# Optimization experiments

Hardware: AMD Instinct MI355X
Metric: run time of the kernel (lower is better)

Reference implementation:

```python
import jax, jax.numpy as jnp
import numpy as np

H = 8
NUM_GRAPHS = 128
EDGE_DIM = 147

def _glorot(k, shape, fan_in):
    return jax.random.normal(k, shape, jnp.float32) * (1.0 / np.sqrt(fan_in))

def setup_inputs():
    ks = jax.random.split(jax.random.key(0), 28)
    N, E = 50000, 200000
    inp = {}
    inp['x'] = jax.random.normal(ks[0], (N, 64), jnp.float32)
    inp['edge_attr'] = jax.random.uniform(ks[1], (E, EDGE_DIM), dtype=jnp.float32)
    dims = [(64, 64), (512, 64), (512, 32)]  # (in_channels, per-head out) per GATConv layer
    ki = 2
    for i in range(3):
        cin, c = dims[i]
        hc = H * c
        inp['W%d' % i] = _glorot(ks[ki], (hc, cin), cin); ki += 1
        inp['We%d' % i] = _glorot(ks[ki], (hc, EDGE_DIM), EDGE_DIM); ki += 1
        inp['as%d' % i] = _glorot(ks[ki], (1, H, c), c); ki += 1
        inp['ad%d' % i] = _glorot(ks[ki], (1, H, c), c); ki += 1
        inp['ae%d' % i] = _glorot(ks[ki], (1, H, c), c); ki += 1
        inp['b%d' % i] = jnp.zeros((hc,), jnp.float32); ki += 1
    inp['Wc'] = _glorot(ks[ki], (32, 256), 256)
    inp['bc'] = jnp.zeros((32,), jnp.float32)
    inp['edge_index'] = jax.random.randint(ks[ki + 1], (2, E), 0, N)
    inp['batch'] = jnp.sort(jax.random.randint(ks[ki + 2], (N,), 0, NUM_GRAPHS))
    return inp

def _gat_layer(x, src, dst, ea, W, We, a_s, a_d, a_e, b):
    # PyG GATConv (concat=True, eval mode): project, per-edge attention logits,
    # softmax over incoming edges of each destination node, weighted scatter-sum, bias.
    N = x.shape[0]
    HC = W.shape[0]
    C = HC // H
    xp = (x @ W.T).reshape(N, H, C)              # [N,H,C]
    ep = (ea @ We.T).reshape(-1, H, C)           # [E,H,C]
    logits = (xp * a_s).sum(-1)[src] + (xp * a_d).sum(-1)[dst] + (ep * a_e).sum(-1)
    logits = jax.nn.leaky_relu(logits, 0.2)      # [E,H]
    mx = jax.ops.segment_max(logits, dst, num_segments=N)
    mx = jnp.where(jnp.isfinite(mx), mx, 0.0)
    ex = jnp.exp(logits - mx[dst])
    denom = jax.ops.segment_sum(ex, dst, num_segments=N)
    attn = ex / (denom[dst] + 1e-16)             # [E,H]
    out = jax.ops.segment_sum(xp[src] * attn[:, :, None], dst, num_segments=N)
    return out.reshape(N, HC) + b

def _forward(x, edge_attr, params, Wc, bc, edge_index, batch):
    N = x.shape[0]
    src, dst = edge_index[0], edge_index[1]
    # GATConv add_self_loops=True, fill_value='mean': self-loop edge attr is
    # the per-node mean of incoming edge attrs (0 for isolated nodes).
    ones_e = jnp.ones((src.shape[0],), x.dtype)
    deg = jax.ops.segment_sum(ones_e, dst, num_segments=N)
    loop_attr = jax.ops.segment_sum(edge_attr, dst, num_segments=N) / jnp.clip(deg, 1.0)[:, None]
    ar = jnp.arange(N)
    src_f = jnp.concatenate([src, ar])
    dst_f = jnp.concatenate([dst, ar])
    ea_f = jnp.concatenate([edge_attr, loop_attr], axis=0)
    h = x
    for i, p in enumerate(params):
        h = _gat_layer(h, src_f, dst_f, ea_f, *p)
        if i < len(params) - 1:
            h = jax.nn.elu(h)  # dropout is identity in eval
    # batch indices are sorted and contiguous, so the unique->contiguous remap
    # in the original forward is the identity; global mean pool:
    cnt = jax.ops.segment_sum(jnp.ones((N,), h.dtype), batch, num_segments=NUM_GRAPHS)
    pooled = jax.ops.segment_sum(h, batch, num_segments=NUM_GRAPHS) / jnp.clip(cnt, 1.0)[:, None]
    return pooled @ Wc.T + bc

def reference(x, edge_attr, W0, We0, as0, ad0, ae0, b0, W1, We1, as1, ad1, ae1, b1, W2, We2, as2, ad2, ae2, b2, Wc, bc, edge_index, batch):
    params = [(W0, We0, as0, ad0, ae0, b0), (W1, We1, as1, ad1, ae1, b1), (W2, We2, as2, ad2, ae2, b2)]
    return _forward(x, edge_attr, params, Wc, bc, edge_index, batch)
```

## Files before the change

kernel.cpp:

```cpp
#include <hip/hip_runtime.h>
#include <hip/hip_bf16.h>
#include <math.h>

typedef __attribute__((ext_vector_type(8))) _Float16 f16x8;
typedef __attribute__((ext_vector_type(4))) _Float16 f16x4;
typedef __attribute__((ext_vector_type(4))) float f32x4;

#define AS1(p) ((const __attribute__((address_space(1))) void*)(p))
#define AS3(p) ((__attribute__((address_space(3))) void*)(p))

__device__ __forceinline__ float leaky02(float x){ return x > 0.f ? x : 0.2f*x; }
__device__ __forceinline__ ushort f2h(float f){ _Float16 h = (_Float16)f; return *(ushort*)&h; }
__device__ __forceinline__ float h2f(ushort u){ _Float16 h = *(_Float16*)&u; return (float)h; }

__global__ void count_kernel(const int* __restrict__ dst, int* __restrict__ cnt, int E){
  int e = blockIdx.x*blockDim.x + threadIdx.x;
  if (e < E) atomicAdd(&cnt[dst[e]], 1);
}

__global__ void scanA_kernel(const int* __restrict__ cnt, int* __restrict__ bsum, int N){
  __shared__ int sd[256];
  int i = blockIdx.x*256 + threadIdx.x;
  sd[threadIdx.x] = (i<N) ? cnt[i] : 0;
  __syncthreads();
  for (int off=128; off>0; off>>=1){
    if (threadIdx.x < off) sd[threadIdx.x] += sd[threadIdx.x+off];
    __syncthreads();
  }
  if (threadIdx.x==0) bsum[blockIdx.x] = sd[0];
}
__global__ void scanB_kernel(int* __restrict__ bsum, int B){
  __shared__ int sd[256];
  int t = threadIdx.x;
  int v = (t<B) ? bsum[t] : 0;
  sd[t] = v;
  __syncthreads();
  for (int off=1; off<256; off<<=1){
    int u = (t>=off) ? sd[t-off] : 0;
    __syncthreads();
    sd[t] += u;
    __syncthreads();
  }
  if (t<B) bsum[t] = sd[t] - v;
}
__global__ void scanC_kernel(const int* __restrict__ cnt, const int* __restrict__ bsum,
                             int* __restrict__ row_ptr, int N){
  __shared__ int sd[256];
  int i = blockIdx.x*256 + threadIdx.x;
  int v = (i<N) ? cnt[i] : 0;
  sd[threadIdx.x] = v;
  __syncthreads();
  for (int off=1; off<256; off<<=1){
    int u = (threadIdx.x>=off) ? sd[threadIdx.x-off] : 0;
    __syncthreads();
    sd[threadIdx.x] += u;
    __syncthreads();
  }
  if (i < N) row_ptr[i+1] = sd[threadIdx.x] + bsum[blockIdx.x];
  if (i == 0) row_ptr[0] = 0;
}

__global__ void scatter_kernel(const int* __restrict__ dst, const int* __restrict__ row_ptr,
                               int* __restrict__ cursor, int* __restrict__ csr, int E){
  int e = blockIdx.x*blockDim.x + threadIdx.x;
  if (e < E){
    int d = dst[e];
    int pos = row_ptr[d] + atomicAdd(&cursor[d], 1);
    csr[pos] = e;
  }
}

__global__ void conv4_kernel(const float* __restrict__ p0, const float* __restrict__ p1,
                             const float* __restrict__ p2, const float* __restrict__ p3,
                             ushort* __restrict__ q0, ushort* __restrict__ q1,
                             ushort* __restrict__ q2, ushort* __restrict__ q3,
                             int n0, int n1, int n2, int n3){
  int i = blockIdx.x*256 + threadIdx.x;
  const float* src; ushort* dst; int loc;
  if (i < n0){ src=p0; dst=q0; loc=i; }
  else if (i < n0+n1){ src=p1; dst=q1; loc=i-n0; }
  else if (i < n0+n1+n2){ src=p2; dst=q2; loc=i-n0-n1; }
  else if (i < n0+n1+n2+n3){ src=p3; dst=q3; loc=i-n0-n1-n2; }
  else return;
  float4 v = reinterpret_cast<const float4*>(src)[loc];
  ushort4 o; o.x=f2h(v.x); o.y=f2h(v.y); o.z=f2h(v.z); o.w=f2h(v.w);
  reinterpret_cast<ushort4*>(dst)[loc] = o;
}

__global__ void wfold_direct_kernel(const float* __restrict__ We0, const float* __restrict__ ae0,
                                    const float* __restrict__ We1, const float* __restrict__ ae1,
                                    const float* __restrict__ We2, const float* __restrict__ ae2,
                                    ushort* __restrict__ Bh){
  int t = blockIdx.x*256 + threadIdx.x;
  if (t >= 32*160) return;
  int j = t/160, d = t%160;
  float s = 0.f;
  if (j < 24 && d < 147){
    int l = j >> 3, h = j & 7;
    const float* We = (l==0) ? We0 : (l==1) ? We1 : We2;
    const float* ae = (l==0) ? ae0 : (l==1) ? ae1 : ae2;
    int C = (l==2) ? 32 : 64;
    for (int c=0;c<C;c++) s = fmaf(We[(size_t)(h*C+c)*147 + d], ae[h*C+c], s);
  }
  Bh[t] = f2h(s);
}

__global__ __launch_bounds__(256) void edge_alpha_mfma_kernel(const float* __restrict__ ea, const ushort* __restrict__ Bh,
                                                              float* __restrict__ alphaE, int E){
  int wave = threadIdx.x>>6, lane = threadIdx.x&63;
  int fr = lane&15, fq = lane>>4;
  int m0 = blockIdx.x*64 + wave*16;
  f32x4 acc0 = {0.f,0.f,0.f,0.f}, acc1 = {0.f,0.f,0.f,0.f};
  int row = m0 + fr; if (row > E-1) row = E-1;
  const float*  ar = ea + (size_t)row*147;
  const ushort* b0 = Bh + (size_t)fr*160      + fq*8;
  const ushort* b1 = Bh + (size_t)(16+fr)*160 + fq*8;
  #pragma unroll
  for (int k=0;k<160;k+=32){
    int c0 = k + fq*8;
    f16x8 a;
    #pragma unroll
    for (int u=0;u<8;u++){
      float v = (c0+u < 147) ? ar[c0+u] : 0.f;
      a[u] = (_Float16)v;
    }
    f16x8 p = *(const f16x8*)(b0 + k);
    f16x8 q = *(const f16x8*)(b1 + k);
    acc0 = __builtin_amdgcn_mfma_f32_16x16x32_f16(a, p, acc0, 0, 0, 0);
    acc1 = __builtin_amdgcn_mfma_f32_16x16x32_f16(a, q, acc1, 0, 0, 0);
  }
  #pragma unroll
  for (int j=0;j<4;j++){
    int r = m0 + fq*4 + j;
    if (r < E){
      alphaE[(size_t)r*24 + fr] = acc0[j];
      if (fr < 8) alphaE[(size_t)r*24 + 16 + fr] = acc1[j];
    }
  }
}

__global__ __launch_bounds__(192) void loop_alpha_all_kernel(const float* __restrict__ alphaE, const int* __restrict__ row_ptr,
                                                             const int* __restrict__ csr, float* __restrict__ loopAE, int N){
  int n = blockIdx.x*8 + threadIdx.x/24;
  int j = threadIdx.x%24;
  if (n >= N) return;
  int row = row_ptr[n], end = row_ptr[n+1];
  float s = 0.f;
  for (int i=row;i<end;i++) s += alphaE[(size_t)csr[i]*24 + j];
  loopAE[(size_t)n*24 + j] = s / fmaxf((float)(end-row), 1.0f);
}

template<int CPH>
__global__ __launch_bounds__(256) void gemm_mfma_kernel(const ushort* __restrict__ A, const ushort* __restrict__ B,
                                                        ushort* __restrict__ C,
                                                        const float* __restrict__ a_s, const float* __restrict__ a_d,
                                                        float* __restrict__ alphaS, float* __restrict__ alphaD,
                                                        int M, int Nn, int K){
  __shared__ ushort As[128*64];
  __shared__ ushort Bs[128*64];
  int m0 = blockIdx.x*128, n0 = blockIdx.y*128;
  int wave = threadIdx.x >> 6, lane = threadIdx.x & 63;
  int wr = wave >> 1, wc = wave & 1;
  f32x4 acc[4][4];
  #pragma unroll
  for (int m=0;m<4;m++)
    #pragma unroll
    for (int n=0;n<4;n++) acc[m][n] = (f32x4){0.f,0.f,0.f,0.f};

  int lrow = lane >> 3;
  int lcol = lane & 7;
  int srcChunk = lcol ^ lrow;
  int fr = lane & 15;
  int fq = lane >> 4;

  for (int k0=0; k0<K; k0+=64){
    #pragma unroll
    for (int q=0;q<4;q++){
      int r = q*32 + wave*8 + lrow;
      int gr = m0 + r; if (gr > M-1) gr = M-1;
      __builtin_amdgcn_global_load_lds(AS1(A + (size_t)gr*K + k0 + srcChunk*8), AS3(&As[(q*32 + wave*8)*64]), 16, 0, 0);
      __builtin_amdgcn_global_load_lds(AS1(B + (size_t)(n0 + r)*K + k0 + srcChunk*8), AS3(&Bs[(q*32 + wave*8)*64]), 16, 0, 0);
    }
    __syncthreads();
    #pragma unroll
    for (int kk=0; kk<64; kk+=32){
      f16x8 a[4], b[4];
      #pragma unroll
      for (int m=0;m<4;m++){
        int Ra = wr*64 + m*16 + fr;
        int ch = ((kk>>3) + fq) ^ (Ra & 7);
        a[m] = *(const f16x8*)&As[Ra*64 + ch*8];
      }
      #pragma unroll
      for (int n=0;n<4;n++){
        int Rb = wc*64 + n*16 + fr;
        int ch = ((kk>>3) + fq) ^ (Rb & 7);
        b[n] = *(const f16x8*)&Bs[Rb*64 + ch*8];
      }
      #pragma unroll
      for (int m=0;m<4;m++)
        #pragma unroll
        for (int n=0;n<4;n++)
          acc[m][n] = __builtin_amdgcn_mfma_f32_16x16x32_f16(a[m], b[n], acc[m][n], 0, 0, 0);
    }
    __syncthreads();
  }
  #pragma unroll
  for (int m=0;m<4;m++){
    #pragma unroll
    for (int j=0;j<4;j++){
      int row = m0 + wr*64 + m*16 + fq*4 + j;
      if (row < M){
        ushort* cp = C + (size_t)row*Nn + n0 + wc*64 + fr;
        #pragma unroll
        for (int n=0;n<4;n++) cp[n*16] = f2h(acc[m][n][j]);
      }
    }
  }
  int colbase = n0 + wc*64;
  if (CPH == 64){
    int head = colbase >> 6;
    float asv[4], adv[4];
    #pragma unroll
    for (int n=0;n<4;n++){ int cih = n*16 + fr; asv[n] = a_s[head*64 + cih]; adv[n] = a_d[head*64 + cih]; }
    #pragma unroll
    for (int m=0;m<4;m++){
      float ps[4] = {0,0,0,0}, pd[4] = {0,0,0,0};
      #pragma unroll
      for (int n=0;n<4;n++)
        #pragma unroll
        for (int j=0;j<4;j++){ ps[j] = fmaf(acc[m][n][j], asv[n], ps[j]); pd[j] = fmaf(acc[m][n][j], adv[n], pd[j]); }
      #pragma unroll
      for (int off=1; off<16; off<<=1)
        #pragma unroll
        for (int j=0;j<4;j++){ ps[j] += __shfl_xor(ps[j], off); pd[j] += __shfl_xor(pd[j], off); }
      if (fr == 0){
        #pragma unroll
        for (int j=0;j<4;j++){
          int row = m0 + wr*64 + m*16 + fq*4 + j;
          if (row < M){ alphaS[(size_t)row*8 + head] = ps[j]; alphaD[(size_t)row*8 + head] = pd[j]; }
        }
      }
    }
  } else {
    int head0 = colbase >> 5;
    float asv[4], adv[4];
    #pragma unroll
    for (int n=0;n<4;n++){
      int h = head0 + (n>>1);
      int cih = (n&1)*16 + fr;
      asv[n] = a_s[h*32 + cih]; adv[n] = a_d[h*32 + cih];
    }
    #pragma unroll
    for (int m=0;m<4;m++){
      float psA[4]={0,0,0,0}, pdA[4]={0,0,0,0}, psB[4]={0,0,0,0}, pdB[4]={0,0,0,0};
      #pragma unroll
      for (int j=0;j<4;j++){
        #pragma unroll
        for (int n=0;n<2;n++){ psA[j] = fmaf(acc[m][n][j], asv[n], psA[j]); pdA[j] = fmaf(acc[m][n][j], adv[n], pdA[j]); }
        #pragma unroll
        for (int n=2;n<4;n++){ psB[j] = fmaf(acc[m][n][j], asv[n], psB[j]); pdB[j] = fmaf(acc[m][n][j], adv[n], pdB[j]); }
      }
      #pragma unroll
      for (int off=1; off<16; off<<=1)
        #pragma unroll
        for (int j=0;j<4;j++){
          psA[j] += __shfl_xor(psA[j], off); pdA[j] += __shfl_xor(pdA[j], off);
          psB[j] += __shfl_xor(psB[j], off); pdB[j] += __shfl_xor(pdB[j], off);
        }
      if (fr == 0){
        #pragma unroll
        for (int j=0;j<4;j++){
          int row = m0 + wr*64 + m*16 + fq*4 + j;
          if (row < M){
            alphaS[(size_t)row*8 + head0]     = psA[j]; alphaD[(size_t)row*8 + head0]     = pdA[j];
            alphaS[(size_t)row*8 + head0 + 1] = psB[j]; alphaD[(size_t)row*8 + head0 + 1] = pdB[j];
          }
        }
      }
    }
  }
}

template<int HC, int ELU>
__global__ __launch_bounds__(256) void aggregate_kernel(
    const ushort* __restrict__ xh, const float* __restrict__ alphaS, const float* __restrict__ alphaD,
    const float* __restrict__ alphaE, const float* __restrict__ loopAE,
    const int* __restrict__ row_ptr, const int* __restrict__ csr, const int* __restrict__ src,
    const float* __restrict__ bias, ushort* __restrict__ out, int N){
  constexpr int V = HC/64;
  int n = blockIdx.x*4 + (threadIdx.x>>6);
  if (n >= N) return;
  int lane = threadIdx.x & 63;
  int h = lane >> 3;
  float adn = alphaD[(size_t)n*8 + h];
  float ls = leaky02(alphaS[(size_t)n*8 + h] + adn + loopAE[(size_t)n*24 + h]);
  float ex = __expf(ls);
  float denom = ex;
  float acc[V];
  {
    const ushort* xr = xh + (size_t)n*HC + V*lane;
    if (V == 8){
      f16x8 v = *(const f16x8*)xr;
      #pragma unroll
      for (int j=0;j<8;j++) acc[j] = ex * (float)v[j];
    } else {
      f16x4 v = *(const f16x4*)xr;
      #pragma unroll
      for (int j=0;j<V;j++) acc[j] = ex * (float)v[j];
    }
  }
  int i1 = row_ptr[n+1];
  for (int i=row_ptr[n]; i<i1; i++){
    int e = csr[i]; int s = src[e];
    float t = leaky02(alphaS[(size_t)s*8 + h] + adn + alphaE[(size_t)e*24 + h]);
    float exv = __expf(t);
    denom += exv;
    const ushort* xs = xh + (size_t)s*HC + V*lane;
    if (V == 8){
      f16x8 v = *(const f16x8*)xs;
      #pragma unroll
      for (int j=0;j<8;j++) acc[j] = fmaf(exv, (float)v[j], acc[j]);
    } else {
      f16x4 v = *(const f16x4*)xs;
      #pragma unroll
      for (int j=0;j<V;j++) acc[j] = fmaf(exv, (float)v[j], acc[j]);
    }
  }
  float inv = 1.f/(denom + 1e-16f);
  if (V == 8){
    f16x8 ov;
    #pragma unroll
    for (int j=0;j<8;j++){
      float o = acc[j]*inv + bias[V*lane + j];
      if (ELU) o = (o > 0.f) ? o : expm1f(o);
      ov[j] = (_Float16)o;
    }
    *(f16x8*)(out + (size_t)n*HC + V*lane) = ov;
  } else {
    f16x4 ov;
    #pragma unroll
    for (int j=0;j<V;j++){
      float o = acc[j]*inv + bias[V*lane + j];
      if (ELU) o = (o > 0.f) ? o : expm1f(o);
      ov[j] = (_Float16)o;
    }
    *(f16x4*)(out + (size_t)n*HC + V*lane) = ov;
  }
}

__global__ __launch_bounds__(256) void pool_sum_kernel(const ushort* __restrict__ h, const int* __restrict__ batch,
                                                       float* __restrict__ pooled, int N){
  __shared__ int bsh[128];
  int i0 = blockIdx.x*128;
  int i1 = min(i0+128, N);
  if (threadIdx.x < i1-i0) bsh[threadIdx.x] = batch[i0+threadIdx.x];
  __syncthreads();
  int c = threadIdx.x;
  int gprev = bsh[0];
  float s = 0.f;
  for (int i=i0;i<i1;i++){
    int g = bsh[i-i0];
    if (g != gprev){ atomicAdd(&pooled[gprev*256 + c], s); s = 0.f; gprev = g; }
    s += h2f(h[(size_t)i*256 + c]);
  }
  atomicAdd(&pooled[gprev*256 + c], s);
}

__device__ __forceinline__ int lower_bound_i(const int* a, int n, int key){
  int lo=0, hi=n;
  while (lo<hi){ int mid=(lo+hi)>>1; if (a[mid]<key) lo=mid+1; else hi=mid; }
  return lo;
}

__global__ void final_kernel(const float* __restrict__ pooled, const int* __restrict__ batch,
                             const float* __restrict__ Wc, const float* __restrict__ bc,
                             float* __restrict__ out, int N){
  int g = blockIdx.x; int j = threadIdx.x;
  if (j >= 32) return;
  int start = lower_bound_i(batch, N, g);
  int end   = lower_bound_i(batch, N, g+1);
  float invc = 1.f / fmaxf((float)(end-start), 1.f);
  const float* p = pooled + g*256;
  const float* w = Wc + (size_t)j*256;
  float s = 0.f;
  for (int c=0;c<256;c++) s = fmaf(p[c], w[c], s);
  out[g*32 + j] = s*invc + bc[j];
}

extern "C" void kernel_launch(void* const* d_in, const int* in_sizes, int n_in,
                              void* d_out, int out_size, void* d_ws, size_t ws_size,
                              hipStream_t stream){
  (void)n_in; (void)out_size; (void)ws_size;
  const float* x   = (const float*)d_in[0];
  const float* ea  = (const float*)d_in[1];
  const float* Wt[3]  = {(const float*)d_in[2],  (const float*)d_in[8],  (const float*)d_in[14]};
  const float* Wet[3] = {(const float*)d_in[3],  (const float*)d_in[9],  (const float*)d_in[15]};
  const float* ast[3] = {(const float*)d_in[4],  (const float*)d_in[10], (const float*)d_in[16]};
  const float* adt[3] = {(const float*)d_in[5],  (const float*)d_in[11], (const float*)d_in[17]};
  const float* aet[3] = {(const float*)d_in[6],  (const float*)d_in[12], (const float*)d_in[18]};
  const float* bt[3]  = {(const float*)d_in[7],  (const float*)d_in[13], (const float*)d_in[19]};
  const float* Wc  = (const float*)d_in[20];
  const float* bc  = (const float*)d_in[21];
  const int* ei    = (const int*)d_in[22];
  const int* batch = (const int*)d_in[23];
  int N = in_sizes[0] / 64;
  int E = in_sizes[1] / 147;
  const int* srcp = ei;
  const int* dstp = ei + E;

  char* w = (char*)d_ws;
  size_t off = 0;
  auto carve = [&](size_t bytes)->char*{ char* p = w + off; off += (bytes + 255) & ~(size_t)255; return p; };
  ushort* xh     = (ushort*)carve((size_t)N*512*2);
  ushort* hb     = (ushort*)carve((size_t)N*512*2);
  ushort* xb     = (ushort*)carve((size_t)N*64*2);
  ushort* Wb[3];
  Wb[0] = (ushort*)carve((size_t)512*64*2);
  Wb[1] = (ushort*)carve((size_t)512*512*2);
  Wb[2] = (ushort*)carve((size_t)256*512*2);
  ushort* wfBh   = (ushort*)carve((size_t)32*160*2);
  float*  alphaE = (float*) carve((size_t)E*24*4);
  float*  loopAE = (float*) carve((size_t)N*24*4);
  float*  alphaS = (float*) carve((size_t)N*8*4);
  float*  alphaD = (float*) carve((size_t)N*8*4);
  int*    row_ptr= (int*)   carve((size_t)(N+1)*4);
  int*    csr    = (int*)   carve((size_t)E*4);
  int*    bsum   = (int*)   carve((size_t)256*4);
  char*   zbase  = carve(0);
  float*  pooled = (float*) carve((size_t)128*256*4);
  int*    cnt    = (int*)   carve((size_t)N*4);
  int*    cursor = (int*)   carve((size_t)N*4);
  char*   zend   = carve(0);

  hipMemsetAsync(zbase, 0, (size_t)(zend - zbase), stream);

  int nscan = (N+255)/256;
  count_kernel  <<<(E+255)/256, 256, 0, stream>>>(dstp, cnt, E);
  scanA_kernel  <<<nscan, 256, 0, stream>>>(cnt, bsum, N);
  scanB_kernel  <<<1, 256, 0, stream>>>(bsum, nscan);
  scanC_kernel  <<<nscan, 256, 0, stream>>>(cnt, bsum, row_ptr, N);
  scatter_kernel<<<(E+255)/256, 256, 0, stream>>>(dstp, row_ptr, cursor, csr, E);

  wfold_direct_kernel<<<(32*160+255)/256, 256, 0, stream>>>(Wet[0], aet[0], Wet[1], aet[1], Wet[2], aet[2], wfBh);

  conv4_kernel<<<(N*16 + 8192 + 65536 + 32768 + 255)/256, 256, 0, stream>>>(
      x, Wt[0], Wt[1], Wt[2], xb, Wb[0], Wb[1], Wb[2], N*16, 8192, 65536, 32768);

  edge_alpha_mfma_kernel<<<(E+63)/64, 256, 0, stream>>>(ea, wfBh, alphaE, E);
  loop_alpha_all_kernel <<<(N+7)/8, 192, 0, stream>>>(alphaE, row_ptr, csr, loopAE, N);

  const int HCs[3]  = {512, 512, 256};
  const int CINs[3] = {64, 512, 512};
  for (int l=0; l<3; l++){
    int HC = HCs[l], CIN = CINs[l];
    const ushort* Ain = (l==0) ? xb : hb;
    dim3 ggrid((N+127)/128, HC/128);
    if (HC==512) gemm_mfma_kernel<64><<<ggrid, 256, 0, stream>>>(Ain, Wb[l], xh, ast[l], adt[l], alphaS, alphaD, N, HC, CIN);
    else         gemm_mfma_kernel<32><<<ggrid, 256, 0, stream>>>(Ain, Wb[l], xh, ast[l], adt[l], alphaS, alphaD, N, HC, CIN);
    int ablocks = (N + 3) / 4;
    if (l==0)
      aggregate_kernel<512,1><<<ablocks, 256, 0, stream>>>(xh, alphaS, alphaD, alphaE + 0*8, loopAE + 0*8, row_ptr, csr, srcp, bt[l], hb, N);
    else if (l==1)
      aggregate_kernel<512,1><<<ablocks, 256, 0, stream>>>(xh, alphaS, alphaD, alphaE + 1*8, loopAE + 1*8, row_ptr, csr, srcp, bt[l], hb, N);
    else
      aggregate_kernel<256,0><<<ablocks, 256, 0, stream>>>(xh, alphaS, alphaD, alphaE + 2*8, loopAE + 2*8, row_ptr, csr, srcp, bt[l], hb, N);
  }
  pool_sum_kernel<<<(N+127)/128, 256, 0, stream>>>(hb, batch, pooled, N);
  final_kernel<<<128, 64, 0, stream>>>(pooled, batch, Wc, bc, (float*)d_out, N);
}
```

Measured before the change: 502.1 us.

## Double-buffer GEMM LDS, swizzle blocks across XCDs, stage output, unroll aggregation

The GEMM kernel now double-buffers its A/B tiles in LDS using async global-to-LDS loads with explicit vmcnt waits, so the next K tile loads while the current one runs on MFMA. It switches to a 1D grid with an XCD-aware block remap so neighbouring tiles share L2, and writes C through LDS to get 16-byte coalesced stores. The aggregate kernel's neighbour loop is unrolled by two so more gathers are in flight. LDS use grows to 64KB per block, which may lower occupancy, and the hand-written waitcnt and barriers are fragile.

```diff
diff --git a/kernel.cpp b/kernel.cpp
--- a/kernel.cpp
+++ b/kernel.cpp
@@ -155,10 +155,15 @@
                                                         ushort* __restrict__ C,
                                                         const float* __restrict__ a_s, const float* __restrict__ a_d,
                                                         float* __restrict__ alphaS, float* __restrict__ alphaD,
-                                                        int M, int Nn, int K){
-  __shared__ ushort As[128*64];
-  __shared__ ushort Bs[128*64];
-  int m0 = blockIdx.x*128, n0 = blockIdx.y*128;
+                                                        int M, int Nn, int K, int NY){
+  __shared__ ushort lds[128*64*4];
+  int nwg = gridDim.x;
+  int bid = blockIdx.x;
+  int q8 = nwg >> 3, r8 = nwg & 7;
+  int xcd = bid & 7, loc = bid >> 3;
+  int swz = (xcd < r8 ? xcd*(q8+1) : r8*(q8+1) + (xcd-r8)*q8) + loc;
+  int m0 = (swz / NY) * 128, n0 = (swz % NY) * 128;
+
   int wave = threadIdx.x >> 6, lane = threadIdx.x & 63;
   int wr = wave >> 1, wc = wave & 1;
   f32x4 acc[4][4];
@@ -173,15 +178,32 @@
   int fr = lane & 15;
   int fq = lane >> 4;
 
-  for (int k0=0; k0<K; k0+=64){
-    #pragma unroll
-    for (int q=0;q<4;q++){
-      int r = q*32 + wave*8 + lrow;
+  auto stage = [&](int buf, int k0){
+    ushort* As = lds + buf*(128*64*2);
+    ushort* Bs = As + 128*64;
+    #pragma unroll
+    for (int qq=0;qq<4;qq++){
+      int r = qq*32 + wave*8 + lrow;
       int gr = m0 + r; if (gr > M-1) gr = M-1;
-      __builtin_amdgcn_global_load_lds(AS1(A + (size_t)gr*K + k0 + srcChunk*8), AS3(&As[(q*32 + wave*8)*64]), 16, 0, 0);
-      __builtin_amdgcn_global_load_lds(AS1(B + (size_t)(n0 + r)*K + k0 + srcChunk*8), AS3(&Bs[(q*32 + wave*8)*64]), 16, 0, 0);
-    }
-    __syncthreads();
+      __builtin_amdgcn_global_load_lds(AS1(A + (size_t)gr*K + k0 + srcChunk*8), AS3(&As[(qq*32 + wave*8)*64]), 16, 0, 0);
+      __builtin_amdgcn_global_load_lds(AS1(B + (size_t)(n0 + r)*K + k0 + srcChunk*8), AS3(&Bs[(qq*32 + wave*8)*64]), 16, 0, 0);
+    }
+  };
+
+  int nt = K >> 6;
+  stage(0, 0);
+  int buf = 0;
+  for (int t=0; t<nt; ++t){
+    if (t+1 < nt){
+      stage(buf^1, (t+1)<<6);
+      asm volatile("s_waitcnt vmcnt(8)" ::: "memory");
+    } else {
+      asm volatile("s_waitcnt vmcnt(0)" ::: "memory");
+    }
+    __builtin_amdgcn_s_barrier();
+    __builtin_amdgcn_sched_barrier(0);
+    const ushort* As = lds + buf*(128*64*2);
+    const ushort* Bs = As + 128*64;
     #pragma unroll
     for (int kk=0; kk<64; kk+=32){
       f16x8 a[4], b[4];
@@ -203,20 +225,33 @@
         for (int n=0;n<4;n++)
           acc[m][n] = __builtin_amdgcn_mfma_f32_16x16x32_f16(a[m], b[n], acc[m][n], 0, 0, 0);
     }
-    __syncthreads();
-  }
-  #pragma unroll
-  for (int m=0;m<4;m++){
-    #pragma unroll
-    for (int j=0;j<4;j++){
-      int row = m0 + wr*64 + m*16 + fq*4 + j;
-      if (row < M){
-        ushort* cp = C + (size_t)row*Nn + n0 + wc*64 + fr;
-        #pragma unroll
-        for (int n=0;n<4;n++) cp[n*16] = f2h(acc[m][n][j]);
+    __builtin_amdgcn_s_barrier();
+    buf ^= 1;
+  }
+
+  {
+    ushort* Cs = lds;
+    #pragma unroll
+    for (int m=0;m<4;m++)
+      #pragma unroll
+      for (int j=0;j<4;j++){
+        int rr = wr*64 + m*16 + fq*4 + j;
+        #pragma unroll
+        for (int n=0;n<4;n++)
+          Cs[rr*128 + wc*64 + n*16 + fr] = f2h(acc[m][n][j]);
       }
-    }
-  }
+    __builtin_amdgcn_s_barrier();
+    int rbase = threadIdx.x >> 4;
+    int cc = (threadIdx.x & 15)*8;
+    #pragma unroll
+    for (int p=0;p<8;p++){
+      int rr = p*16 + rbase;
+      int grow = m0 + rr;
+      if (grow < M)
+        *(f16x8*)(C + (size_t)grow*Nn + n0 + cc) = *(const f16x8*)&Cs[rr*128 + cc];
+    }
+  }
+
   int colbase = n0 + wc*64;
   if (CPH == 64){
     int head = colbase >> 6;
@@ -310,8 +345,33 @@
       for (int j=0;j<V;j++) acc[j] = ex * (float)v[j];
     }
   }
-  int i1 = row_ptr[n+1];
-  for (int i=row_ptr[n]; i<i1; i++){
+  int i = row_ptr[n], i1 = row_ptr[n+1];
+  for (; i+1 < i1; i += 2){
+    int e0 = csr[i], e1 = csr[i+1];
+    int s0 = src[e0], s1 = src[e1];
+    float aS0 = alphaS[(size_t)s0*8 + h], aE0 = alphaE[(size_t)e0*24 + h];
+    float aS1 = alphaS[(size_t)s1*8 + h], aE1 = alphaE[(size_t)e1*24 + h];
+    const ushort* x0 = xh + (size_t)s0*HC + V*lane;
+    const ushort* x1 = xh + (size_t)s1*HC + V*lane;
+    if (V == 8){
+      f16x8 v0 = *(const f16x8*)x0;
+      f16x8 v1 = *(const f16x8*)x1;
+      float ex0 = __expf(leaky02(aS0 + adn + aE0));
+      float ex1 = __expf(leaky02(aS1 + adn + aE1));
+      denom += ex0 + ex1;
+      #pragma unroll
+      for (int j=0;j<8;j++) acc[j] = fmaf(ex1, (float)v1[j], fmaf(ex0, (float)v0[j], acc[j]));
+    } else {
+      f16x4 v0 = *(const f16x4*)x0;
+      f16x4 v1 = *(const f16x4*)x1;
+      float ex0 = __expf(leaky02(aS0 + adn + aE0));
+      float ex1 = __expf(leaky02(aS1 + adn + aE1));
+      denom += ex0 + ex1;
+      #pragma unroll
+      for (int j=0;j<V;j++) acc[j] = fmaf(ex1, (float)v1[j], fmaf(ex0, (float)v0[j], acc[j]));
+    }
+  }
+  if (i < i1){
     int e = csr[i]; int s = src[e];
     float t = leaky02(alphaS[(size_t)s*8 + h] + adn + alphaE[(size_t)e*24 + h]);
     float exv = __expf(t);
@@ -452,12 +512,14 @@
 
   const int HCs[3]  = {512, 512, 256};
   const int CINs[3] = {64, 512, 512};
+  int nrow = (N+127)/128;
   for (int l=0; l<3; l++){
     int HC = HCs[l], CIN = CINs[l];
     const ushort* Ain = (l==0) ? xb : hb;
-    dim3 ggrid((N+127)/128, HC/128);
-    if (HC==512) gemm_mfma_kernel<64><<<ggrid, 256, 0, stream>>>(Ain, Wb[l], xh, ast[l], adt[l], alphaS, alphaD, N, HC, CIN);
-    else         gemm_mfma_kernel<32><<<ggrid, 256, 0, stream>>>(Ain, Wb[l], xh, ast[l], adt[l], alphaS, alphaD, N, HC, CIN);
+    int NY = HC/128;
+    int nwg = nrow * NY;
+    if (HC==512) gemm_mfma_kernel<64><<<nwg, 256, 0, stream>>>(Ain, Wb[l], xh, ast[l], adt[l], alphaS, alphaD, N, HC, CIN, NY);
+    else         gemm_mfma_kernel<32><<<nwg, 256, 0, stream>>>(Ain, Wb[l], xh, ast[l], adt[l], alphaS, alphaD, N, HC, CIN, NY);
     int ablocks = (N + 3) / 4;
     if (l==0)
       aggregate_kernel<512,1><<<ablocks, 256, 0, stream>>>(xh, alphaS, alphaD, alphaE + 0*8, loopAE + 0*8, row_ptr, csr, srcp, bt[l], hb, N);
```

Measured after the change: 476.7 us. 1.05x faster.
